# Optimization experiments

Measured on AMD Instinct MI355X. Metric: run time of the kernel, lower is better.

Reference implementation:

```python
import jax, jax.numpy as jnp
import numpy as np

RES = (160, 160, 160)            # (X, Y, Z)
AABB_MIN, AABB_MAX = -1.3, 1.3
DEG = 2
SH_DIM = (DEG + 1) ** 2          # 9
N_SAMPLES = 480                  # 'plenoxels': mean(res)*3*voxel_mul
NEAR, FAR = 0.2, 6.0
WHITE_BKGD = True
N_RAYS = 2048

C0 = 0.28209479177387814
C1 = 0.4886025119029199
C2 = (1.0925484305920792, -1.0925484305920792, 0.31539156525252005,
      -1.0925484305920792, 0.5462742152960396)


def sh_encoder(dirs):
    # real spherical harmonics up to degree 2 of the normalized view dir
    d = dirs / jnp.linalg.norm(dirs, axis=-1, keepdims=True)
    x, y, z = d[..., 0], d[..., 1], d[..., 2]
    return jnp.stack([
        jnp.full_like(x, C0),
        -C1 * y, C1 * z, -C1 * x,
        C2[0] * x * y, C2[1] * y * z,
        C2[2] * (2.0 * z * z - x * x - y * y),
        C2[3] * x * z, C2[4] * (x * x - y * y),
    ], axis=-1)                                     # [..., 9]


def trilinear_sample(grid, coords):
    # grid: [C, X, Y, Z]; coords: [..., 3] in (-1, 1).
    # torch F.grid_sample convention: coord x indexes last dim (Z), y -> Y, z -> X.
    # align_corners=True, padding_mode='zeros'.
    Cc, X, Y, Z = grid.shape
    gf = grid.reshape(Cc, -1)
    fx = (coords[..., 0] + 1.0) * 0.5 * (Z - 1)
    fy = (coords[..., 1] + 1.0) * 0.5 * (Y - 1)
    fz = (coords[..., 2] + 1.0) * 0.5 * (X - 1)
    x0f = jnp.floor(fx); y0f = jnp.floor(fy); z0f = jnp.floor(fz)
    wx = fx - x0f; wy = fy - y0f; wz = fz - z0f
    x0 = x0f.astype(jnp.int32); y0 = y0f.astype(jnp.int32); z0 = z0f.astype(jnp.int32)
    out = jnp.zeros(coords.shape[:-1] + (Cc,), dtype=grid.dtype)
    for dz in (0, 1):
        for dy in (0, 1):
            for dx in (0, 1):
                ix = x0 + dx; iy = y0 + dy; iz = z0 + dz
                valid = ((ix >= 0) & (ix < Z) & (iy >= 0) & (iy < Y)
                         & (iz >= 0) & (iz < X))
                w = ((wx if dx else 1.0 - wx)
                     * (wy if dy else 1.0 - wy)
                     * (wz if dz else 1.0 - wz)) * valid
                lin = (jnp.clip(iz, 0, X - 1) * Y + jnp.clip(iy, 0, Y - 1)) * Z \
                      + jnp.clip(ix, 0, Z - 1)
                vals = jnp.take(gf, lin, axis=1)    # [C, ...]
                out = out + jnp.moveaxis(vals, 0, -1) * w[..., None]
    return out                                      # [..., C]


def get_intersections(rays_o, rays_d, aabb, step, n):
    off_pos = (aabb[1] - rays_o) / rays_d
    off_neg = (aabb[0] - rays_o) / rays_d
    start = jnp.max(jnp.minimum(off_pos, off_neg), axis=-1, keepdims=True)
    start = jnp.clip(start, NEAR, FAR)
    steps = jnp.arange(n, dtype=rays_o.dtype)[None, :]
    return start + steps * step                     # [N, n]


def setup_inputs() -> dict:
    key = jax.random.key(0)
    k1, k2, k3, k4 = jax.random.split(key, 4)
    rays_o = jax.random.normal(k1, (N_RAYS, 3), jnp.float32) * 0.1   # inside aabb
    rays_d = jax.random.normal(k2, (N_RAYS, 3), jnp.float32)
    sigma_data = 0.1 + 0.05 * jax.random.normal(k3, (1,) + RES, jnp.float32)
    rgb_data = 0.01 * jax.random.normal(k4, (3 * SH_DIM,) + RES, jnp.float32)
    return {"rays_o": rays_o, "rays_d": rays_d,
            "sigma_data": sigma_data, "rgb_data": rgb_data}


def reference(rays_o, rays_d, sigma_data, rgb_data):
    dt = rays_o.dtype
    aabb = jnp.array([[AABB_MIN] * 3, [AABB_MAX] * 3], dtype=dt)
    aabb_size = aabb[1] - aabb[0]
    inv_aabb_size = 2.0 / aabb_size
    step = jnp.linalg.norm(aabb_size) / N_SAMPLES   # voxel_len

    inter = jax.lax.stop_gradient(
        get_intersections(rays_o, rays_d, aabb, step, N_SAMPLES))  # [N,S]
    pts = rays_o[:, None, :] + rays_d[:, None, :] * inter[:, :-1, None]  # [N,S-1,3]
    pn = (pts - aabb[0]) * inv_aabb_size - 1.0       # normalized (-1,1)

    sigma = jax.nn.relu(trilinear_sample(sigma_data, pn)[..., 0])   # [N,S-1]

    dists = jnp.diff(inter, axis=1) * jnp.linalg.norm(rays_d, axis=-1, keepdims=True)
    alpha = 1.0 - jnp.exp(-sigma * dists)
    cum_light = jnp.concatenate(
        [jnp.ones((alpha.shape[0], 1), dtype=dt),
         jnp.cumprod(1.0 - alpha[:, :-1] + 1e-10, axis=-1)], axis=-1)
    abs_light = alpha * cum_light                    # [N,S-1]

    sh_mult = sh_encoder(rays_d)                     # [N,9]
    rgb_feat = trilinear_sample(rgb_data, pn)        # [N,S-1,27]
    rgb_feat = rgb_feat.reshape(rgb_feat.shape[0], rgb_feat.shape[1], 3, SH_DIM)
    sh_rgb = jnp.einsum('nsck,nk->nsc', rgb_feat, sh_mult)

    rgb = jax.nn.sigmoid(sh_rgb)
    rgb_map = jnp.einsum('ns,nsc->nc', abs_light, rgb)
    if WHITE_BKGD:
        rgb_map = rgb_map + (1.0 - abs_light.sum(-1, keepdims=True))
    return rgb_map
```

## Files before the change

### kernel.cpp

```cpp
#include <hip/hip_runtime.h>
#include <math.h>

#define RESN  160
#define VOX   4096000
#define YSTR  160
#define ZSTR  25600
#define NPTS  478
#define NRAYS 2048
#define REC   32

typedef float f2_u __attribute__((ext_vector_type(2), aligned(4)));

__global__ __launch_bounds__(256)
void transpose_grid(const float* __restrict__ sig, const float* __restrict__ rgb,
                    unsigned short* __restrict__ rec)
{
    const int v = blockIdx.x * 256 + threadIdx.x;
    float vals[32];
    vals[0] = sig[v];
    #pragma unroll
    for (int k = 0; k < 27; ++k) vals[1 + k] = rgb[(size_t)k * VOX + v];
    vals[28] = vals[29] = vals[30] = vals[31] = 0.f;
    unsigned short h[32];
    #pragma unroll
    for (int k = 0; k < 32; ++k) {
        unsigned u = __float_as_uint(vals[k]);
        unsigned r = (u + 0x7FFFu + ((u >> 16) & 1u)) >> 16;
        h[k] = (unsigned short)r;
    }
    uint4* dst = (uint4*)(rec + (size_t)v * REC);
    const uint4* src = (const uint4*)h;
    #pragma unroll
    for (int i = 0; i < 4; ++i) dst[i] = src[i];
}

__device__ __forceinline__ void bf2(unsigned u, float& lo, float& hi) {
    lo = __uint_as_float(u << 16);
    hi = __uint_as_float(u & 0xFFFF0000u);
}

__global__ __launch_bounds__(256)
void plenoxel_render2(const float* __restrict__ rays_o,
                      const float* __restrict__ rays_d,
                      const unsigned short* __restrict__ rec,
                      float* __restrict__ out)
{
    const int ray  = blockIdx.x;
    const int tid  = threadIdx.x;
    const int wave = tid >> 6;
    const int lane = tid & 63;

    const float ox = rays_o[ray*3+0], oy = rays_o[ray*3+1], oz = rays_o[ray*3+2];
    const float dxr = rays_d[ray*3+0], dyr = rays_d[ray*3+1], dzr = rays_d[ray*3+2];

    const float h = 2.6f * 1.7320508075688772f / 480.0f;

    const float ax = (1.3f - ox) / dxr, bx = (-1.3f - ox) / dxr;
    const float ay = (1.3f - oy) / dyr, by = (-1.3f - oy) / dyr;
    const float az = (1.3f - oz) / dzr, bz = (-1.3f - oz) / dzr;
    float start = fmaxf(fmaxf(fminf(ax, bx), fminf(ay, by)), fminf(az, bz));
    start = fminf(fmaxf(start, 0.2f), 6.0f);

    const float B = 1.3164f;
    const float mx1 = ( B - ox) / dxr, mx0 = (-B - ox) / dxr;
    const float my1 = ( B - oy) / dyr, my0 = (-B - oy) / dyr;
    const float mz1 = ( B - oz) / dzr, mz0 = (-B - oz) / dzr;
    float tl = fmaxf(fmaxf(fminf(mx0, mx1), fminf(my0, my1)), fminf(mz0, mz1));
    float th = fminf(fminf(fmaxf(mx0, mx1), fmaxf(my0, my1)), fmaxf(mz0, mz1));
    tl = fmaxf(tl, start);
    th = fminf(th, fmaf((float)NPTS, h, start));
    int s_lo, s_hi;
    if (th < tl) { s_lo = 0; s_hi = -1; }
    else {
        s_lo = max(0,    (int)floorf((tl - start) / h) - 1);
        s_hi = min(NPTS, (int)ceilf ((th - start) / h) + 1);
    }

    const float dsq  = dxr*dxr + dyr*dyr + dzr*dzr;
    const float dinv = rsqrtf(dsq);
    const float dn   = sqrtf(dsq);
    const float X = dxr * dinv, Y = dyr * dinv, Z = dzr * dinv;
    const float shv[9] = {
        0.28209479177387814f,
        -0.4886025119029199f * Y,
         0.4886025119029199f * Z,
        -0.4886025119029199f * X,
         1.0925484305920792f * X * Y,
        -1.0925484305920792f * Y * Z,
         0.31539156525252005f * (2.0f * Z * Z - X * X - Y * Y),
        -1.0925484305920792f * X * Z,
         0.5462742152960396f * (X * X - Y * Y),
    };
    const float dist = h * dn;

    float accR = 0.f, accG = 0.f, accB = 0.f, accL = 0.f;
    float carry = 1.0f;

    const int nlive = s_hi - s_lo + 1;
    if (nlive > 0) {
        const int chunk = (nlive + 3) >> 2;
        const int my_lo = s_lo + wave * chunk;
        const int my_hi = min(my_lo + chunk - 1, s_hi);

        for (int basei = my_lo; basei <= my_hi; basei += 64) {
            const int s = basei + lane;
            float alpha = 0.f, cr = 0.f, cg = 0.f, cb = 0.f;
            if (s <= my_hi) {
                const float t  = fmaf((float)s, h, start);
                const float px = fmaf(dxr, t, ox);
                const float py = fmaf(dyr, t, oy);
                const float pz = fmaf(dzr, t, oz);
                const float fx = fmaf(px, 61.153846153846f, 79.5f);
                const float fy = fmaf(py, 61.153846153846f, 79.5f);
                const float fz = fmaf(pz, 61.153846153846f, 79.5f);
                const float fxf = floorf(fx), fyf = floorf(fy), fzf = floorf(fz);
                const int   x0 = (int)fxf, y0 = (int)fyf, z0 = (int)fzf;
                const float wx1 = fx - fxf, wy1 = fy - fyf, wz1 = fz - fzf;
                const float wx0 = 1.f - wx1, wy0 = 1.f - wy1, wz0 = 1.f - wz1;

                float sv = 0.f, a0 = 0.f, a1 = 0.f, a2 = 0.f;

                if (x0 >= 0 && x0 <= 158 && y0 >= 0 && y0 <= 158 && z0 >= 0 && z0 <= 158) {
                    const float wzy[4] = { wz0*wy0, wz0*wy1, wz1*wy0, wz1*wy1 };
                    const int   offp[4] = { 0, YSTR*REC, ZSTR*REC, (ZSTR+YSTR)*REC };
                    const size_t base = ((size_t)z0 * ZSTR + (size_t)y0 * YSTR + x0) * REC;
                    #pragma unroll
                    for (int p = 0; p < 4; ++p) {
                        const uint4* P = (const uint4*)(rec + base + offp[p]);
                        uint4 q0[4], q1[4];
                        q0[0]=P[0]; q0[1]=P[1]; q0[2]=P[2]; q0[3]=P[3];
                        q1[0]=P[4]; q1[1]=P[5]; q1[2]=P[6]; q1[3]=P[7];
                        const float wA = wzy[p] * wx0, wB = wzy[p] * wx1;
                        #pragma unroll
                        for (int q = 0; q < 4; ++q) {
                            const unsigned* u0 = (const unsigned*)&q0[q];
                            const unsigned* u1 = (const unsigned*)&q1[q];
                            #pragma unroll
                            for (int d = 0; d < 4; ++d) {
                                const int ch = q*8 + d*2;
                                if (ch >= 28) break;
                                float l0, h0, l1, h1;
                                bf2(u0[d], l0, h0);
                                bf2(u1[d], l1, h1);
                                const float vA = fmaf(l1, wB, l0 * wA);
                                const float vBv= fmaf(h1, wB, h0 * wA);
                                if (ch == 0) sv += vA;
                                else {
                                    const int j = ch - 1;
                                    const float c = shv[j % 9] * vA;
                                    if (j < 9) a0 += c; else if (j < 18) a1 += c; else a2 += c;
                                }
                                if (ch + 1 < 28) {
                                    const int j = ch;
                                    const float c = shv[j % 9] * vBv;
                                    if (j < 9) a0 += c; else if (j < 18) a1 += c; else a2 += c;
                                }
                            }
                        }
                    }
                } else {
                    const float vwx[2] = { (x0   >= 0 && x0   < RESN) ? wx0 : 0.f,
                                           (x0+1 >= 0 && x0+1 < RESN) ? wx1 : 0.f };
                    const float vwy[2] = { (y0   >= 0 && y0   < RESN) ? wy0 : 0.f,
                                           (y0+1 >= 0 && y0+1 < RESN) ? wy1 : 0.f };
                    const float vwz[2] = { (z0   >= 0 && z0   < RESN) ? wz0 : 0.f,
                                           (z0+1 >= 0 && z0+1 < RESN) ? wz1 : 0.f };
                    const int cx[2] = { min(max(x0,0),RESN-1), min(max(x0+1,0),RESN-1) };
                    const int cy[2] = { min(max(y0,0),RESN-1), min(max(y0+1,0),RESN-1) };
                    const int cz[2] = { min(max(z0,0),RESN-1), min(max(z0+1,0),RESN-1) };
                    for (int dz = 0; dz < 2; ++dz)
                    for (int dy = 0; dy < 2; ++dy)
                    for (int dx = 0; dx < 2; ++dx) {
                        const float w = vwz[dz]*vwy[dy]*vwx[dx];
                        if (w == 0.f) continue;
                        const uint4* P = (const uint4*)(rec +
                            ((size_t)cz[dz]*ZSTR + (size_t)cy[dy]*YSTR + cx[dx]) * REC);
                        uint4 qq[4]; qq[0]=P[0]; qq[1]=P[1]; qq[2]=P[2]; qq[3]=P[3];
                        #pragma unroll
                        for (int q = 0; q < 4; ++q) {
                            const unsigned* u = (const unsigned*)&qq[q];
                            #pragma unroll
                            for (int d = 0; d < 4; ++d) {
                                const int ch = q*8 + d*2;
                                if (ch >= 28) break;
                                float lo, hi; bf2(u[d], lo, hi);
                                if (ch == 0) sv = fmaf(lo, w, sv);
                                else {
                                    const int j = ch - 1;
                                    const float c = shv[j % 9] * lo * w;
                                    if (j < 9) a0 += c; else if (j < 18) a1 += c; else a2 += c;
                                }
                                if (ch + 1 < 28) {
                                    const int j = ch;
                                    const float c = shv[j % 9] * hi * w;
                                    if (j < 9) a0 += c; else if (j < 18) a1 += c; else a2 += c;
                                }
                            }
                        }
                    }
                }

                sv = fmaxf(sv, 0.f);
                alpha = 1.f - __expf(-sv * dist);
                cr = __fdividef(1.f, 1.f + __expf(-a0));
                cg = __fdividef(1.f, 1.f + __expf(-a1));
                cb = __fdividef(1.f, 1.f + __expf(-a2));
            }

            float m = (s <= my_hi) ? (1.f - alpha + 1e-10f) : 1.f;
            float incl = m;
            #pragma unroll
            for (int off = 1; off < 64; off <<= 1) {
                float nb = __shfl_up(incl, off);
                if (lane >= off) incl *= nb;
            }
            float excl = __shfl_up(incl, 1);
            if (lane == 0) excl = 1.f;

            const float T = carry * excl;
            const float w = T * alpha;
            accR = fmaf(w, cr, accR);
            accG = fmaf(w, cg, accG);
            accB = fmaf(w, cb, accB);
            accL += w;
            carry *= __shfl(incl, 63);
        }
    }

    #pragma unroll
    for (int off = 32; off; off >>= 1) {
        accR += __shfl_xor(accR, off);
        accG += __shfl_xor(accG, off);
        accB += __shfl_xor(accB, off);
        accL += __shfl_xor(accL, off);
    }

    __shared__ float sP[4], sR[4], sG[4], sB[4], sL[4];
    if (lane == 0) { sP[wave]=carry; sR[wave]=accR; sG[wave]=accG; sB[wave]=accB; sL[wave]=accL; }
    __syncthreads();
    if (tid == 0) {
        float T = 1.f, R = 0.f, G = 0.f, Bc = 0.f, L = 0.f;
        #pragma unroll
        for (int w = 0; w < 4; ++w) {
            R  += T * sR[w];
            G  += T * sG[w];
            Bc += T * sB[w];
            L  += T * sL[w];
            T  *= sP[w];
        }
        const float bg = 1.f - L;
        out[ray*3+0] = R  + bg;
        out[ray*3+1] = G  + bg;
        out[ray*3+2] = Bc + bg;
    }
}

__device__ __forceinline__ float plane_interior(const float* __restrict__ p,
                                                float w00, float w01, float w10, float w11,
                                                float wx0, float wx1)
{
    f2_u a = *(const f2_u*)(p);
    f2_u b = *(const f2_u*)(p + YSTR);
    f2_u c = *(const f2_u*)(p + ZSTR);
    f2_u d = *(const f2_u*)(p + ZSTR + YSTR);
    float v0 = fmaf(a.y, wx1, a.x * wx0);
    float v1 = fmaf(b.y, wx1, b.x * wx0);
    float v2 = fmaf(c.y, wx1, c.x * wx0);
    float v3 = fmaf(d.y, wx1, d.x * wx0);
    return fmaf(v3, w11, fmaf(v2, w10, fmaf(v1, w01, v0 * w00)));
}

__global__ __launch_bounds__(64)
void plenoxel_render_f32(const float* __restrict__ rays_o,
                         const float* __restrict__ rays_d,
                         const float* __restrict__ sig,
                         const float* __restrict__ rgb,
                         float* __restrict__ out)
{
    const int ray  = blockIdx.x;
    const int lane = threadIdx.x;
    const float ox = rays_o[ray*3+0], oy = rays_o[ray*3+1], oz = rays_o[ray*3+2];
    const float dxr = rays_d[ray*3+0], dyr = rays_d[ray*3+1], dzr = rays_d[ray*3+2];
    const float h = 2.6f * 1.7320508075688772f / 480.0f;
    const float ax = (1.3f - ox) / dxr, bx = (-1.3f - ox) / dxr;
    const float ay = (1.3f - oy) / dyr, by = (-1.3f - oy) / dyr;
    const float az = (1.3f - oz) / dzr, bz = (-1.3f - oz) / dzr;
    float start = fmaxf(fmaxf(fminf(ax, bx), fminf(ay, by)), fminf(az, bz));
    start = fminf(fmaxf(start, 0.2f), 6.0f);
    const float B = 1.3164f;
    const float mx1 = ( B - ox) / dxr, mx0 = (-B - ox) / dxr;
    const float my1 = ( B - oy) / dyr, my0 = (-B - oy) / dyr;
    const float mz1 = ( B - oz) / dzr, mz0 = (-B - oz) / dzr;
    float tl = fmaxf(fmaxf(fminf(mx0, mx1), fminf(my0, my1)), fminf(mz0, mz1));
    float th = fminf(fminf(fmaxf(mx0, mx1), fmaxf(my0, my1)), fmaxf(mz0, mz1));
    tl = fmaxf(tl, start);
    th = fminf(th, fmaf((float)NPTS, h, start));
    int s_lo, s_hi;
    if (th < tl) { s_lo = 0; s_hi = -1; }
    else {
        s_lo = max(0,    (int)floorf((tl - start) / h) - 1);
        s_hi = min(NPTS, (int)ceilf ((th - start) / h) + 1);
    }
    const float dsq  = dxr*dxr + dyr*dyr + dzr*dzr;
    const float dinv = rsqrtf(dsq);
    const float dn   = sqrtf(dsq);
    const float X = dxr * dinv, Y = dyr * dinv, Z = dzr * dinv;
    const float shv[9] = {
        0.28209479177387814f, -0.4886025119029199f * Y, 0.4886025119029199f * Z,
        -0.4886025119029199f * X, 1.0925484305920792f * X * Y, -1.0925484305920792f * Y * Z,
        0.31539156525252005f * (2.0f * Z * Z - X * X - Y * Y),
        -1.0925484305920792f * X * Z, 0.5462742152960396f * (X * X - Y * Y),
    };
    const float dist = h * dn;
    float accR = 0.f, accG = 0.f, accB = 0.f, accL = 0.f;
    float carry = 1.0f;
    for (int basei = s_lo; basei <= s_hi; basei += 64) {
        const int s = basei + lane;
        float alpha = 0.f, cr = 0.f, cg = 0.f, cb = 0.f;
        if (s <= s_hi) {
            const float t  = fmaf((float)s, h, start);
            const float px = fmaf(dxr, t, ox);
            const float py = fmaf(dyr, t, oy);
            const float pz = fmaf(dzr, t, oz);
            const float fx = fmaf(px, 61.153846153846f, 79.5f);
            const float fy = fmaf(py, 61.153846153846f, 79.5f);
            const float fz = fmaf(pz, 61.153846153846f, 79.5f);
            const float fxf = floorf(fx), fyf = floorf(fy), fzf = floorf(fz);
            const int   x0 = (int)fxf, y0 = (int)fyf, z0 = (int)fzf;
            const float wx1 = fx - fxf, wy1 = fy - fyf, wz1 = fz - fzf;
            const float wx0 = 1.f - wx1, wy0 = 1.f - wy1, wz0 = 1.f - wz1;
            float sv = 0.f, a0 = 0.f, a1 = 0.f, a2 = 0.f;
            if (x0 >= 0 && x0 <= 158 && y0 >= 0 && y0 <= 158 && z0 >= 0 && z0 <= 158) {
                const float w00 = wz0*wy0, w01 = wz0*wy1, w10 = wz1*wy0, w11 = wz1*wy1;
                const size_t bofs = (size_t)z0 * ZSTR + (size_t)y0 * YSTR + (size_t)x0;
                sv = plane_interior(sig + bofs, w00, w01, w10, w11, wx0, wx1);
                const float* rp = rgb + bofs;
                #pragma unroll
                for (int c = 0; c < 3; ++c) {
                    float sc = 0.f;
                    #pragma unroll
                    for (int k = 0; k < 9; ++k) {
                        const float v = plane_interior(rp + (size_t)(c*9+k)*VOX,
                                                       w00, w01, w10, w11, wx0, wx1);
                        sc = fmaf(v, shv[k], sc);
                    }
                    if (c == 0) a0 = sc; else if (c == 1) a1 = sc; else a2 = sc;
                }
            } else {
                const float vwx0 = (x0   >= 0 && x0   < RESN) ? wx0 : 0.f;
                const float vwx1 = (x0+1 >= 0 && x0+1 < RESN) ? wx1 : 0.f;
                const float vwy0 = (y0   >= 0 && y0   < RESN) ? wy0 : 0.f;
                const float vwy1 = (y0+1 >= 0 && y0+1 < RESN) ? wy1 : 0.f;
                const float vwz0 = (z0   >= 0 && z0   < RESN) ? wz0 : 0.f;
                const float vwz1 = (z0+1 >= 0 && z0+1 < RESN) ? wz1 : 0.f;
                const int cx0 = min(max(x0,   0), RESN-1), cx1 = min(max(x0+1, 0), RESN-1);
                const int cy0 = min(max(y0,   0), RESN-1), cy1 = min(max(y0+1, 0), RESN-1);
                const int cz0 = min(max(z0,   0), RESN-1), cz1 = min(max(z0+1, 0), RESN-1);
                const float cw[8] = { vwz0*vwy0*vwx0, vwz0*vwy0*vwx1,
                                      vwz0*vwy1*vwx0, vwz0*vwy1*vwx1,
                                      vwz1*vwy0*vwx0, vwz1*vwy0*vwx1,
                                      vwz1*vwy1*vwx0, vwz1*vwy1*vwx1 };
                const size_t co[8] = {
                    (size_t)cz0*ZSTR + (size_t)cy0*YSTR + cx0,
                    (size_t)cz0*ZSTR + (size_t)cy0*YSTR + cx1,
                    (size_t)cz0*ZSTR + (size_t)cy1*YSTR + cx0,
                    (size_t)cz0*ZSTR + (size_t)cy1*YSTR + cx1,
                    (size_t)cz1*ZSTR + (size_t)cy0*YSTR + cx0,
                    (size_t)cz1*ZSTR + (size_t)cy0*YSTR + cx1,
                    (size_t)cz1*ZSTR + (size_t)cy1*YSTR + cx0,
                    (size_t)cz1*ZSTR + (size_t)cy1*YSTR + cx1 };
                #pragma unroll
                for (int j = 0; j < 8; ++j) {
                    if (cw[j] != 0.f) {
                        const float wj = cw[j];
                        sv = fmaf(sig[co[j]], wj, sv);
                        const float* rp = rgb + co[j];
                        float t0 = 0.f, t1 = 0.f, t2 = 0.f;
                        #pragma unroll
                        for (int k = 0; k < 9; ++k) {
                            t0 = fmaf(rp[(size_t)(k     )*VOX], shv[k], t0);
                            t1 = fmaf(rp[(size_t)(k +  9)*VOX], shv[k], t1);
                            t2 = fmaf(rp[(size_t)(k + 18)*VOX], shv[k], t2);
                        }
                        a0 = fmaf(t0, wj, a0);
                        a1 = fmaf(t1, wj, a1);
                        a2 = fmaf(t2, wj, a2);
                    }
                }
            }
            sv = fmaxf(sv, 0.f);
            alpha = 1.f - __expf(-sv * dist);
            cr = __fdividef(1.f, 1.f + __expf(-a0));
            cg = __fdividef(1.f, 1.f + __expf(-a1));
            cb = __fdividef(1.f, 1.f + __expf(-a2));
        }
        float m = (s <= s_hi) ? (1.f - alpha + 1e-10f) : 1.f;
        float incl = m;
        #pragma unroll
        for (int off = 1; off < 64; off <<= 1) {
            float nb = __shfl_up(incl, off);
            if (lane >= off) incl *= nb;
        }
        float excl = __shfl_up(incl, 1);
        if (lane == 0) excl = 1.f;
        const float T = carry * excl;
        const float w = T * alpha;
        accR = fmaf(w, cr, accR);
        accG = fmaf(w, cg, accG);
        accB = fmaf(w, cb, accB);
        accL += w;
        carry *= __shfl(incl, 63);
    }
    #pragma unroll
    for (int off = 32; off; off >>= 1) {
        accR += __shfl_xor(accR, off);
        accG += __shfl_xor(accG, off);
        accB += __shfl_xor(accB, off);
        accL += __shfl_xor(accL, off);
    }
    if (lane == 0) {
        const float bg = 1.f - accL;
        out[ray*3+0] = accR + bg;
        out[ray*3+1] = accG + bg;
        out[ray*3+2] = accB + bg;
    }
}

extern "C" void kernel_launch(void* const* d_in, const int* in_sizes, int n_in,
                              void* d_out, int out_size, void* d_ws, size_t ws_size,
                              hipStream_t stream) {
    const float* rays_o = (const float*)d_in[0];
    const float* rays_d = (const float*)d_in[1];
    const float* sig    = (const float*)d_in[2];
    const float* rgb    = (const float*)d_in[3];
    float* out = (float*)d_out;

    const size_t need = (size_t)VOX * REC * sizeof(unsigned short);
    if (ws_size >= need) {
        unsigned short* rec = (unsigned short*)d_ws;
        transpose_grid<<<VOX / 256, 256, 0, stream>>>(sig, rgb, rec);
        plenoxel_render2<<<NRAYS, 256, 0, stream>>>(rays_o, rays_d, rec, out);
    } else {
        plenoxel_render_f32<<<NRAYS, 64, 0, stream>>>(rays_o, rays_d, sig, rgb, out);
    }
}
```

Measured before the change: 667.3 us.

## Halve waves per ray and split interior corner loads into two register batches

The render kernel now uses 128 threads (two waves) per ray instead of four, so each wave handles a longer chunk of samples. The interior trilinear path loads the first half of each corner's record for all four planes, processes it, then loads and processes the second half, which cuts the number of live registers holding loaded data. The intent is higher occupancy and better load batching. In exchange there is less parallelism per ray and the scan loop runs more serial iterations per wave.

New measurement: 669.3 us. Within noise of the previous version (+0.3%).

```diff
diff --git a/kernel.cpp b/kernel.cpp
--- a/kernel.cpp
+++ b/kernel.cpp
@@ -39,8 +39,20 @@
     hi = __uint_as_float(u & 0xFFFF0000u);
 }
 
-__global__ __launch_bounds__(256)
-void plenoxel_render2(const float* __restrict__ rays_o,
+#define ROUTE(slot, val)                                              \
+    do {                                                              \
+        if ((slot) == 0) sv += (val);                                 \
+        else if ((slot) < 28) {                                       \
+            const int _j = (slot) - 1;                                \
+            const float _c = shv[_j % 9] * (val);                     \
+            if (_j < 9) a0 += _c;                                     \
+            else if (_j < 18) a1 += _c;                               \
+            else a2 += _c;                                            \
+        }                                                             \
+    } while (0)
+
+__global__ __launch_bounds__(128)
+void plenoxel_render3(const float* __restrict__ rays_o,
                       const float* __restrict__ rays_d,
                       const unsigned short* __restrict__ rec,
                       float* __restrict__ out)
@@ -98,7 +110,7 @@
 
     const int nlive = s_hi - s_lo + 1;
     if (nlive > 0) {
-        const int chunk = (nlive + 3) >> 2;
+        const int chunk = (nlive + 1) >> 1;
         const int my_lo = s_lo + wave * chunk;
         const int my_hi = min(my_lo + chunk - 1, s_hi);
 
@@ -122,38 +134,66 @@
 
                 if (x0 >= 0 && x0 <= 158 && y0 >= 0 && y0 <= 158 && z0 >= 0 && z0 <= 158) {
                     const float wzy[4] = { wz0*wy0, wz0*wy1, wz1*wy0, wz1*wy1 };
-                    const int   offp[4] = { 0, YSTR*REC, ZSTR*REC, (ZSTR+YSTR)*REC };
                     const size_t base = ((size_t)z0 * ZSTR + (size_t)y0 * YSTR + x0) * REC;
-                    #pragma unroll
-                    for (int p = 0; p < 4; ++p) {
-                        const uint4* P = (const uint4*)(rec + base + offp[p]);
-                        uint4 q0[4], q1[4];
-                        q0[0]=P[0]; q0[1]=P[1]; q0[2]=P[2]; q0[3]=P[3];
-                        q1[0]=P[4]; q1[1]=P[5]; q1[2]=P[6]; q1[3]=P[7];
-                        const float wA = wzy[p] * wx0, wB = wzy[p] * wx1;
-                        #pragma unroll
-                        for (int q = 0; q < 4; ++q) {
-                            const unsigned* u0 = (const unsigned*)&q0[q];
-                            const unsigned* u1 = (const unsigned*)&q1[q];
+                    const uint4* P0 = (const uint4*)(rec + base);
+                    const uint4* P1 = (const uint4*)(rec + base + (size_t)YSTR*REC);
+                    const uint4* P2 = (const uint4*)(rec + base + (size_t)ZSTR*REC);
+                    const uint4* P3 = (const uint4*)(rec + base + (size_t)(ZSTR+YSTR)*REC);
+                    const uint4* PP[4] = { P0, P1, P2, P3 };
+
+                    {
+                        uint4 r0[4][2], r1[4][2];
+                        #pragma unroll
+                        for (int p = 0; p < 4; ++p) {
+                            r0[p][0] = PP[p][0]; r0[p][1] = PP[p][1];
+                            r1[p][0] = PP[p][4]; r1[p][1] = PP[p][5];
+                        }
+                        #pragma unroll
+                        for (int p = 0; p < 4; ++p) {
+                            const float wA = wzy[p] * wx0, wB = wzy[p] * wx1;
                             #pragma unroll
-                            for (int d = 0; d < 4; ++d) {
-                                const int ch = q*8 + d*2;
-                                if (ch >= 28) break;
-                                float l0, h0, l1, h1;
-                                bf2(u0[d], l0, h0);
-                                bf2(u1[d], l1, h1);
-                                const float vA = fmaf(l1, wB, l0 * wA);
-                                const float vBv= fmaf(h1, wB, h0 * wA);
-                                if (ch == 0) sv += vA;
-                                else {
-                                    const int j = ch - 1;
-                                    const float c = shv[j % 9] * vA;
-                                    if (j < 9) a0 += c; else if (j < 18) a1 += c; else a2 += c;
+                            for (int q = 0; q < 2; ++q) {
+                                const unsigned* u0 = (const unsigned*)&r0[p][q];
+                                const unsigned* u1 = (const unsigned*)&r1[p][q];
+                                #pragma unroll
+                                for (int d = 0; d < 4; ++d) {
+                                    const int slot = q*8 + d*2;
+                                    float l0, h0, l1, h1;
+                                    bf2(u0[d], l0, h0);
+                                    bf2(u1[d], l1, h1);
+                                    const float vA = fmaf(l1, wB, l0 * wA);
+                                    const float vB2 = fmaf(h1, wB, h0 * wA);
+                                    ROUTE(slot, vA);
+                                    ROUTE(slot + 1, vB2);
                                 }
-                                if (ch + 1 < 28) {
-                                    const int j = ch;
-                                    const float c = shv[j % 9] * vBv;
-                                    if (j < 9) a0 += c; else if (j < 18) a1 += c; else a2 += c;
+                            }
+                        }
+                    }
+                    {
+                        uint4 r0[4][2], r1[4][2];
+                        #pragma unroll
+                        for (int p = 0; p < 4; ++p) {
+                            r0[p][0] = PP[p][2]; r0[p][1] = PP[p][3];
+                            r1[p][0] = PP[p][6]; r1[p][1] = PP[p][7];
+                        }
+                        #pragma unroll
+                        for (int p = 0; p < 4; ++p) {
+                            const float wA = wzy[p] * wx0, wB = wzy[p] * wx1;
+                            #pragma unroll
+                            for (int q = 0; q < 2; ++q) {
+                                const unsigned* u0 = (const unsigned*)&r0[p][q];
+                                const unsigned* u1 = (const unsigned*)&r1[p][q];
+                                #pragma unroll
+                                for (int d = 0; d < 4; ++d) {
+                                    const int slot = 16 + q*8 + d*2;
+                                    if (slot >= 28) break;
+                                    float l0, h0, l1, h1;
+                                    bf2(u0[d], l0, h0);
+                                    bf2(u1[d], l1, h1);
+                                    const float vA = fmaf(l1, wB, l0 * wA);
+                                    const float vB2 = fmaf(h1, wB, h0 * wA);
+                                    ROUTE(slot, vA);
+                                    ROUTE(slot + 1, vB2);
                                 }
                             }
                         }
@@ -181,20 +221,11 @@
                             const unsigned* u = (const unsigned*)&qq[q];
                             #pragma unroll
                             for (int d = 0; d < 4; ++d) {
-                                const int ch = q*8 + d*2;
-                                if (ch >= 28) break;
+                                const int slot = q*8 + d*2;
+                                if (slot >= 28) break;
                                 float lo, hi; bf2(u[d], lo, hi);
-                                if (ch == 0) sv = fmaf(lo, w, sv);
-                                else {
-                                    const int j = ch - 1;
-                                    const float c = shv[j % 9] * lo * w;
-                                    if (j < 9) a0 += c; else if (j < 18) a1 += c; else a2 += c;
-                                }
-                                if (ch + 1 < 28) {
-                                    const int j = ch;
-                                    const float c = shv[j % 9] * hi * w;
-                                    if (j < 9) a0 += c; else if (j < 18) a1 += c; else a2 += c;
-                                }
+                                ROUTE(slot, lo * w);
+                                if (slot + 1 < 28) ROUTE(slot + 1, hi * w);
                             }
                         }
                     }
@@ -235,13 +266,13 @@
         accL += __shfl_xor(accL, off);
     }
 
-    __shared__ float sP[4], sR[4], sG[4], sB[4], sL[4];
+    __shared__ float sP[2], sR[2], sG[2], sB[2], sL[2];
     if (lane == 0) { sP[wave]=carry; sR[wave]=accR; sG[wave]=accG; sB[wave]=accB; sL[wave]=accL; }
     __syncthreads();
     if (tid == 0) {
         float T = 1.f, R = 0.f, G = 0.f, Bc = 0.f, L = 0.f;
         #pragma unroll
-        for (int w = 0; w < 4; ++w) {
+        for (int w = 0; w < 2; ++w) {
             R  += T * sR[w];
             G  += T * sG[w];
             Bc += T * sB[w];
@@ -439,7 +470,7 @@
     if (ws_size >= need) {
         unsigned short* rec = (unsigned short*)d_ws;
         transpose_grid<<<VOX / 256, 256, 0, stream>>>(sig, rgb, rec);
-        plenoxel_render2<<<NRAYS, 256, 0, stream>>>(rays_o, rays_d, rec, out);
+        plenoxel_render3<<<NRAYS, 128, 0, stream>>>(rays_o, rays_d, rec, out);
     } else {
         plenoxel_render_f32<<<NRAYS, 64, 0, stream>>>(rays_o, rays_d, sig, rgb, out);
     }
```
